# Optimization experiments

Hardware: AMD Instinct MI355X
Metric: run time of the kernel (lower is better)

Reference implementation:

```python
import jax, jax.numpy as jnp
import numpy as np

S, B, H, T = 512, 64, 512, 32

def setup_inputs() -> dict:
    key = jax.random.key(0)
    ks = jax.random.split(key, 6)
    hidden = jax.random.normal(ks[0], (S, B, H), jnp.float32)
    lens = jax.random.randint(ks[1], (B,), 1, S + 1)  # sentence lengths in [1, S]
    masks = jnp.ones((S, B), jnp.bool_)  # unused (attention is None), kept for signature parity
    W1 = jax.random.normal(ks[2], (H, H), jnp.float32) / np.sqrt(H)
    b1 = jnp.zeros((H,), jnp.float32)
    W2 = jax.random.normal(ks[3], (H, T), jnp.float32) / np.sqrt(H)
    b2 = jnp.zeros((T,), jnp.float32)
    # xavier_normal_ init for transition
    transition = jax.random.normal(ks[4], (T, T), jnp.float32) * np.sqrt(2.0 / (T + T))
    return {"hidden": hidden, "lens": lens, "masks": masks,
            "W1": W1, "b1": b1, "W2": W2, "b2": b2, "transition": transition}


def _viterbi(emissions, lens, transition):
    # emissions: [S, B, T]; transition[curr, prev]
    Sdim, Bdim, Tn = emissions.shape
    ident = jnp.broadcast_to(jnp.arange(Tn), (Bdim, Tn))  # identity backpointers for padded steps

    def step(fv, inp):
        em_t, t = inp
        scores = fv[:, None, :] + transition[None, :, :]  # [B, curr, prev]
        bp = jnp.argmax(scores, axis=-1)                  # [B, T]
        new_fv = jnp.max(scores, axis=-1) + em_t          # [B, T]
        active = (t < lens)[:, None]
        fv = jnp.where(active, new_fv, fv)                # freeze state past sentence end
        bp = jnp.where(active, bp, ident)
        return fv, bp

    fv0 = emissions[0]
    ts = jnp.arange(1, Sdim)
    fv, bps = jax.lax.scan(step, fv0, (emissions[1:], ts))  # bps: [S-1, B, T]
    best_id = jnp.argmax(fv, axis=-1)   # [B]
    best_score = jnp.max(fv, axis=-1)   # [B]

    def back(tag, bp_t):
        prev = jnp.take_along_axis(bp_t, tag[:, None], axis=1)[:, 0]
        return prev, prev

    _, prevs = jax.lax.scan(back, best_id, bps, reverse=True)  # [S-1, B]
    paths = jnp.concatenate([prevs, best_id[None]], axis=0)    # [S, B]; beyond len-1 the tag repeats
    return paths, best_score


def reference(hidden, lens, masks, W1, b1, W2, b2, transition):
    # hidden2emission: Linear -> Sigmoid -> Linear
    h1 = jax.nn.sigmoid(hidden @ W1 + b1)   # [S, B, H]
    emissions = h1 @ W2 + b2                # [S, B, T]
    paths, best_score = _viterbi(emissions, lens, transition)
    return paths, best_score
```

## Files before the change

### kernel.cpp

```cpp
#include <hip/hip_runtime.h>
#include <math.h>

#define SDIM 512
#define BDIM 64
#define HDIM 512
#define TDIM 32
#define MTOT (SDIM * BDIM)

typedef __attribute__((ext_vector_type(8))) short bf16x8;
typedef __attribute__((ext_vector_type(4))) float f32x4;

__device__ unsigned short g_w1hT[HDIM * HDIM];
__device__ unsigned short g_w1lT[HDIM * HDIM];
__device__ unsigned short g_w2hT[TDIM * HDIM];
__device__ unsigned short g_w2lT[TDIM * HDIM];
__device__ float g_em[(size_t)MTOT * TDIM];

__device__ __forceinline__ unsigned short f2bf(float x) {
  union { float f; unsigned int u; } v; v.f = x;
  unsigned int r = v.u + 0x7FFFu + ((v.u >> 16) & 1u);
  return (unsigned short)(r >> 16);
}
__device__ __forceinline__ float bf2f(unsigned short h) {
  union { float f; unsigned int u; } v; v.u = ((unsigned int)h) << 16; return v.f;
}
__device__ __forceinline__ float fmax3(float a, float b, float c) {
  return fmaxf(fmaxf(a, b), c);
}
__device__ __forceinline__ int imin3(int a, int b, int c) {
  int m = a < b ? a : b; return m < c ? m : c;
}

__global__ void split_kernel(const float* __restrict__ W1, const float* __restrict__ W2) {
  const int n = blockIdx.x;
  const int k0 = threadIdx.x * 4;
  if (n < HDIM) {
    ushort4 h, l; float x;
    x = W1[(size_t)(k0 + 0) * HDIM + n]; h.x = f2bf(x); l.x = f2bf(x - bf2f(h.x));
    x = W1[(size_t)(k0 + 1) * HDIM + n]; h.y = f2bf(x); l.y = f2bf(x - bf2f(h.y));
    x = W1[(size_t)(k0 + 2) * HDIM + n]; h.z = f2bf(x); l.z = f2bf(x - bf2f(h.z));
    x = W1[(size_t)(k0 + 3) * HDIM + n]; h.w = f2bf(x); l.w = f2bf(x - bf2f(h.w));
    *(ushort4*)&g_w1hT[(size_t)n * HDIM + k0] = h;
    *(ushort4*)&g_w1lT[(size_t)n * HDIM + k0] = l;
  } else {
    const int t = n - HDIM;
    ushort4 h, l; float x;
    x = W2[(size_t)(k0 + 0) * TDIM + t]; h.x = f2bf(x); l.x = f2bf(x - bf2f(h.x));
    x = W2[(size_t)(k0 + 1) * TDIM + t]; h.y = f2bf(x); l.y = f2bf(x - bf2f(h.y));
    x = W2[(size_t)(k0 + 2) * TDIM + t]; h.z = f2bf(x); l.z = f2bf(x - bf2f(h.z));
    x = W2[(size_t)(k0 + 3) * TDIM + t]; h.w = f2bf(x); l.w = f2bf(x - bf2f(h.w));
    *(ushort4*)&g_w2hT[(size_t)t * HDIM + k0] = h;
    *(ushort4*)&g_w2lT[(size_t)t * HDIM + k0] = l;
  }
}

__global__ __launch_bounds__(256) void emis_kernel(
    const float* __restrict__ hidden, const float* __restrict__ b1,
    const float* __restrict__ b2)
{
  __shared__ unsigned short lAh[64][40];
  __shared__ unsigned short lAl[64][40];
  __shared__ unsigned short lBh[128][40];
  __shared__ unsigned short lBl[128][40];
  __shared__ unsigned short H1h[64][136];
  __shared__ unsigned short H1l[64][136];

  const int tid = threadIdx.x;
  const int s = blockIdx.x;
  const int row0 = s * 64;
  const int wave = tid >> 6;
  const int lane = tid & 63;
  const int l15 = lane & 15;
  const int l4 = lane >> 4;
  const int wr1 = (wave >> 1) * 32;
  const int wc1 = (wave & 1) * 64;

  f32x4 acc_em[2];
  acc_em[0] = (f32x4)(0.f);
  acc_em[1] = (f32x4)(0.f);

  for (int jcb = 0; jcb < 4; ++jcb) {
    const int jc = jcb * 128;

    f32x4 acc1[2][4];
#pragma unroll
    for (int i = 0; i < 2; ++i)
#pragma unroll
      for (int j = 0; j < 4; ++j) acc1[i][j] = (f32x4)(0.f);

    for (int k0 = 0; k0 < HDIM; k0 += 32) {
#pragma unroll
      for (int i = 0; i < 2; ++i) {
        int f4 = tid + 256 * i;
        int r = f4 >> 3, q = f4 & 7;
        float4 v = *(const float4*)&hidden[(size_t)(row0 + r) * HDIM + k0 + 4 * q];
        ushort4 h, l;
        h.x = f2bf(v.x); l.x = f2bf(v.x - bf2f(h.x));
        h.y = f2bf(v.y); l.y = f2bf(v.y - bf2f(h.y));
        h.z = f2bf(v.z); l.z = f2bf(v.z - bf2f(h.z));
        h.w = f2bf(v.w); l.w = f2bf(v.w - bf2f(h.w));
        *(ushort4*)&lAh[r][4 * q] = h;
        *(ushort4*)&lAl[r][4 * q] = l;
      }
#pragma unroll
      for (int i = 0; i < 2; ++i) {
        int f8 = tid + 256 * i;
        int nl = f8 >> 2, kq8 = f8 & 3;
        *(uint4*)&lBh[nl][8 * kq8] =
            *(const uint4*)&g_w1hT[(size_t)(jc + nl) * HDIM + k0 + 8 * kq8];
        *(uint4*)&lBl[nl][8 * kq8] =
            *(const uint4*)&g_w1lT[(size_t)(jc + nl) * HDIM + k0 + 8 * kq8];
      }
      __syncthreads();

      bf16x8 aH[2], aL[2];
#pragma unroll
      for (int i = 0; i < 2; ++i) {
        aH[i] = *(const bf16x8*)&lAh[wr1 + 16 * i + l15][8 * l4];
        aL[i] = *(const bf16x8*)&lAl[wr1 + 16 * i + l15][8 * l4];
      }
#pragma unroll
      for (int j = 0; j < 4; ++j) {
        bf16x8 bH = *(const bf16x8*)&lBh[wc1 + 16 * j + l15][8 * l4];
        bf16x8 bL = *(const bf16x8*)&lBl[wc1 + 16 * j + l15][8 * l4];
#pragma unroll
        for (int i = 0; i < 2; ++i) {
          acc1[i][j] = __builtin_amdgcn_mfma_f32_16x16x32_bf16(aH[i], bH, acc1[i][j], 0, 0, 0);
          acc1[i][j] = __builtin_amdgcn_mfma_f32_16x16x32_bf16(aH[i], bL, acc1[i][j], 0, 0, 0);
          acc1[i][j] = __builtin_amdgcn_mfma_f32_16x16x32_bf16(aL[i], bH, acc1[i][j], 0, 0, 0);
        }
      }
      __syncthreads();
    }

#pragma unroll
    for (int j = 0; j < 4; ++j) {
      const int col = wc1 + 16 * j + l15;
      const float bv = b1[jc + col];
#pragma unroll
      for (int i = 0; i < 2; ++i) {
#pragma unroll
        for (int r = 0; r < 4; ++r) {
          int lrow = wr1 + 16 * i + 4 * l4 + r;
          float h = 1.f / (1.f + expf(-(acc1[i][j][r] + bv)));
          unsigned short hh = f2bf(h);
          unsigned short hl = f2bf(h - bf2f(hh));
          H1h[lrow][col] = hh;
          H1l[lrow][col] = hl;
        }
      }
    }
    __syncthreads();

#pragma unroll
    for (int ks = 0; ks < 4; ++ks) {
      bf16x8 aH2 = *(const bf16x8*)&H1h[16 * wave + l15][32 * ks + 8 * l4];
      bf16x8 aL2 = *(const bf16x8*)&H1l[16 * wave + l15][32 * ks + 8 * l4];
#pragma unroll
      for (int j2 = 0; j2 < 2; ++j2) {
        const size_t wo = (size_t)(16 * j2 + l15) * HDIM + jc + 32 * ks + 8 * l4;
        bf16x8 bH2 = *(const bf16x8*)&g_w2hT[wo];
        bf16x8 bL2 = *(const bf16x8*)&g_w2lT[wo];
        acc_em[j2] = __builtin_amdgcn_mfma_f32_16x16x32_bf16(aH2, bH2, acc_em[j2], 0, 0, 0);
        acc_em[j2] = __builtin_amdgcn_mfma_f32_16x16x32_bf16(aH2, bL2, acc_em[j2], 0, 0, 0);
        acc_em[j2] = __builtin_amdgcn_mfma_f32_16x16x32_bf16(aL2, bH2, acc_em[j2], 0, 0, 0);
      }
    }
    __syncthreads();
  }

#pragma unroll
  for (int j2 = 0; j2 < 2; ++j2) {
    const int t = 16 * j2 + l15;
    const float bv = b2[t];
#pragma unroll
    for (int r = 0; r < 4; ++r) {
      int b = 16 * wave + 4 * l4 + r;
      g_em[((size_t)b * SDIM + s) * TDIM + t] = acc_em[j2][r] + bv;
    }
  }
}

__global__ __launch_bounds__(64) void viterbi_kernel(
    const int* __restrict__ lens, const float* __restrict__ trans,
    float* __restrict__ out)
{
  __shared__ float fvL[64];
  __shared__ unsigned int bps32[SDIM / 4][TDIM];
  const int b = blockIdx.x;
  const int lane = threadIdx.x;
  const int c = lane & 31;
  const int h = lane >> 5;
  const int p0 = 16 * h;

  float tr[16];
#pragma unroll
  for (int j = 0; j < 16; j += 4) {
    float4 t4 = *(const float4*)&trans[c * TDIM + p0 + j];
    tr[j] = t4.x; tr[j + 1] = t4.y; tr[j + 2] = t4.z; tr[j + 3] = t4.w;
  }

  int len;
  { const int* p32 = lens;
    len = (p32[1] == 0) ? (int)((const long long*)lens)[b] : p32[b]; }

  const float* emc = g_em + (size_t)b * SDIM * TDIM + c;

  float fvown = emc[0];
  fvL[lane] = fvown;

  float ebuf[12];
#pragma unroll
  for (int j = 0; j < 12; ++j) ebuf[j] = emc[(size_t)(1 + j) * TDIM];

  unsigned int bpk = 0u;

#define VSTEP(T, PH, EV)                                                       \
  {                                                                            \
    float4 q0 = *(const float4*)&fvL[p0];                                      \
    float4 q1 = *(const float4*)&fvL[p0 + 4];                                  \
    float4 q2 = *(const float4*)&fvL[p0 + 8];                                  \
    float4 q3 = *(const float4*)&fvL[p0 + 12];                                 \
    float sv[16];                                                              \
    sv[0] = q0.x + tr[0];  sv[1] = q0.y + tr[1];                               \
    sv[2] = q0.z + tr[2];  sv[3] = q0.w + tr[3];                               \
    sv[4] = q1.x + tr[4];  sv[5] = q1.y + tr[5];                               \
    sv[6] = q1.z + tr[6];  sv[7] = q1.w + tr[7];                               \
    sv[8] = q2.x + tr[8];  sv[9] = q2.y + tr[9];                               \
    sv[10] = q2.z + tr[10]; sv[11] = q2.w + tr[11];                            \
    sv[12] = q3.x + tr[12]; sv[13] = q3.y + tr[13];                            \
    sv[14] = q3.z + tr[14]; sv[15] = q3.w + tr[15];                            \
    float l0 = fmax3(sv[0], sv[1], sv[2]);                                     \
    float l1 = fmax3(sv[3], sv[4], sv[5]);                                     \
    float l2 = fmax3(sv[6], sv[7], sv[8]);                                     \
    float l3 = fmax3(sv[9], sv[10], sv[11]);                                   \
    float l4 = fmax3(sv[12], sv[13], sv[14]);                                  \
    float mh = fmaxf(fmax3(l0, l1, l2), fmax3(l3, l4, sv[15]));                \
    float mo = __shfl_xor(mh, 32, 64);                                         \
    float m0 = fmaxf(mh, mo);                                                  \
    const bool act = (T) < len;                                                \
    fvown = act ? (m0 + (EV)) : fvown;                                         \
    fvL[lane] = fvown;       \
    int i_[16];                                                                \
    _Pragma("unroll")                                                          \
    for (int j = 0; j < 16; ++j) i_[j] = (sv[j] == m0) ? j : 63;               \
    int u0 = imin3(i_[0], i_[1], i_[2]);                                       \
    int u1 = imin3(i_[3], i_[4], i_[5]);                                       \
    int u2 = imin3(i_[6], i_[7], i_[8]);                                       \
    int u3 = imin3(i_[9], i_[10], i_[11]);                                     \
    int u4 = imin3(i_[12], i_[13], i_[14]);                                    \
    int jm = imin3(imin3(u0, u1, u2), imin3(u3, u4, i_[15]), 63);              \
    int gi = (jm == 63) ? 255 : (p0 + jm);                                     \
    int go = __shfl_xor(gi, 32, 64);                                           \
    int im = gi < go ? gi : go;                                                \
    int bp = act ? im : c;                                                     \
    bpk |= (unsigned)bp << (8 * (PH));                                         \
    if ((PH) == 3) { bps32[(T) >> 2][c] = bpk; bpk = 0u; }                     \
  }

#define LOADQ(BASE, T0)                                                        \
  {                                                                            \
    _Pragma("unroll")                                                          \
    for (int j = 0; j < 4; ++j) {                                              \
      int lt = (T0) + j; lt = lt > (SDIM - 1) ? (SDIM - 1) : lt;               \
      ebuf[(BASE) + j] = emc[(size_t)lt * TDIM];                               \
    }                                                                          \
  }

  {
    int tq = 1;
    for (; tq <= SDIM - 19; tq += 12) {
      VSTEP(tq + 0, 1, ebuf[0]) VSTEP(tq + 1, 2, ebuf[1])
      VSTEP(tq + 2, 3, ebuf[2]) VSTEP(tq + 3, 0, ebuf[3])
      LOADQ(0, tq + 12)
      VSTEP(tq + 4, 1, ebuf[4]) VSTEP(tq + 5, 2, ebuf[5])
      VSTEP(tq + 6, 3, ebuf[6]) VSTEP(tq + 7, 0, ebuf[7])
      LOADQ(4, tq + 16)
      VSTEP(tq + 8, 1, ebuf[8]) VSTEP(tq + 9, 2, ebuf[9])
      VSTEP(tq + 10, 3, ebuf[10]) VSTEP(tq + 11, 0, ebuf[11])
      LOADQ(8, tq + 20)
    }
    VSTEP(505, 1, ebuf[0]) VSTEP(506, 2, ebuf[1]) VSTEP(507, 3, ebuf[2])
    VSTEP(508, 0, ebuf[3]) VSTEP(509, 1, ebuf[4]) VSTEP(510, 2, ebuf[5])
    VSTEP(511, 3, ebuf[6])
  }
#undef VSTEP
#undef LOADQ

  float bs = fvown;
  int bi = c;
#pragma unroll
  for (int off = 16; off > 0; off >>= 1) {
    float os = __shfl_down(bs, off, 32);
    int oi = __shfl_down(bi, off, 32);
    if (os > bs || (os == bs && oi < bi)) { bs = os; bi = oi; }
  }
  bs = __shfl(bs, 0, 32);
  int tag = __shfl(bi, 0, 32);

  out[(size_t)SDIM * BDIM + b] = bs;
  out[(size_t)(SDIM - 1) * BDIM + b] = (float)tag;

  unsigned bw_next = bps32[SDIM / 4 - 1][c];
  for (int w = SDIM / 4 - 1; w >= 0; --w) {
    unsigned bw = bw_next;
    if (w > 0) bw_next = bps32[w - 1][c];
#pragma unroll
    for (int j = 3; j >= 0; --j) {
      int t = 4 * w + j;
      if (t < 1) continue;
      unsigned word = (unsigned)__builtin_amdgcn_readlane((int)bw, tag);
      tag = (int)((word >> (8 * j)) & 255u);
      out[(size_t)(t - 1) * BDIM + b] = (float)tag;
    }
  }
}

static int find_by_size(const int* in_sizes, int n_in, int sz, int fb) {
  for (int i = 0; i < n_in; ++i) if (in_sizes[i] == sz) return i;
  return fb;
}

extern "C" void kernel_launch(void* const* d_in, const int* in_sizes, int n_in,
                              void* d_out, int out_size, void* d_ws, size_t ws_size,
                              hipStream_t stream) {
  const int i_hidden = find_by_size(in_sizes, n_in, SDIM * BDIM * HDIM, 0);
  const int i_lens   = find_by_size(in_sizes, n_in, BDIM, 1);
  const int i_W1     = find_by_size(in_sizes, n_in, HDIM * HDIM, 3);
  const int i_b1     = find_by_size(in_sizes, n_in, HDIM, 4);
  const int i_W2     = find_by_size(in_sizes, n_in, HDIM * TDIM, 5);
  const int i_b2     = find_by_size(in_sizes, n_in, TDIM, 6);
  const int i_tr     = find_by_size(in_sizes, n_in, TDIM * TDIM, 7);

  const float* hidden = (const float*)d_in[i_hidden];
  const int*   lens   = (const int*)d_in[i_lens];
  const float* W1     = (const float*)d_in[i_W1];
  const float* b1     = (const float*)d_in[i_b1];
  const float* W2     = (const float*)d_in[i_W2];
  const float* b2     = (const float*)d_in[i_b2];
  const float* trans  = (const float*)d_in[i_tr];
  float* out = (float*)d_out;

  split_kernel<<<HDIM + TDIM, 128, 0, stream>>>(W1, W2);
  emis_kernel<<<SDIM, 256, 0, stream>>>(hidden, b1, b2);
  viterbi_kernel<<<BDIM, 64, 0, stream>>>(lens, trans, out);
}
```

Baseline: 239.4 us.

## Fuse emission GEMM and Viterbi into one kernel with per-timestep ready flags

Merges the emission kernel and the Viterbi kernel into a single launch. The first 512 blocks compute emissions per timestep and publish a per-timestep flag. Another 16 blocks each run four Viterbi waves that spin on those flags before loading emissions, so decoding overlaps the GEMM instead of waiting for it to finish. It also swaps expf for __expf. This relies on the Viterbi blocks not starving the producer blocks, since they are launched in the same grid, and it enlarges shared memory per block to 65KB, which may lower emission-block occupancy.

Result: slower. 519.2 us (+116.9%).

```diff
diff --git a/kernel.cpp b/kernel.cpp
--- a/kernel.cpp
+++ b/kernel.cpp
@@ -15,6 +15,7 @@
 __device__ unsigned short g_w2hT[TDIM * HDIM];
 __device__ unsigned short g_w2lT[TDIM * HDIM];
 __device__ float g_em[(size_t)MTOT * TDIM];
+__device__ unsigned int g_flag[SDIM];
 
 __device__ __forceinline__ unsigned short f2bf(float x) {
   union { float f; unsigned int u; } v; v.f = x;
@@ -29,6 +30,17 @@
 }
 __device__ __forceinline__ int imin3(int a, int b, int c) {
   int m = a < b ? a : b; return m < c ? m : c;
+}
+__device__ __forceinline__ void wait_flag(int s) {
+  while (__hip_atomic_load(&g_flag[s], __ATOMIC_ACQUIRE,
+                           __HIP_MEMORY_SCOPE_AGENT) == 0u) {
+    __builtin_amdgcn_s_sleep(2);
+  }
+}
+
+__global__ void init_flags() {
+  int i = blockIdx.x * blockDim.x + threadIdx.x;
+  if (i < SDIM) g_flag[i] = 0u;
 }
 
 __global__ void split_kernel(const float* __restrict__ W1, const float* __restrict__ W2) {
@@ -54,173 +66,184 @@
   }
 }
 
-__global__ __launch_bounds__(256) void emis_kernel(
+__global__ __launch_bounds__(256) void fused_kernel(
     const float* __restrict__ hidden, const float* __restrict__ b1,
-    const float* __restrict__ b2)
+    const float* __restrict__ b2, const int* __restrict__ lens,
+    const float* __restrict__ trans, float* __restrict__ out)
 {
-  __shared__ unsigned short lAh[64][40];
-  __shared__ unsigned short lAl[64][40];
-  __shared__ unsigned short lBh[128][40];
-  __shared__ unsigned short lBl[128][40];
-  __shared__ unsigned short H1h[64][136];
-  __shared__ unsigned short H1l[64][136];
-
-  const int tid = threadIdx.x;
-  const int s = blockIdx.x;
-  const int row0 = s * 64;
-  const int wave = tid >> 6;
-  const int lane = tid & 63;
-  const int l15 = lane & 15;
-  const int l4 = lane >> 4;
-  const int wr1 = (wave >> 1) * 32;
-  const int wc1 = (wave & 1) * 64;
-
-  f32x4 acc_em[2];
-  acc_em[0] = (f32x4)(0.f);
-  acc_em[1] = (f32x4)(0.f);
-
-  for (int jcb = 0; jcb < 4; ++jcb) {
-    const int jc = jcb * 128;
-
-    f32x4 acc1[2][4];
-#pragma unroll
-    for (int i = 0; i < 2; ++i)
-#pragma unroll
-      for (int j = 0; j < 4; ++j) acc1[i][j] = (f32x4)(0.f);
-
-    for (int k0 = 0; k0 < HDIM; k0 += 32) {
-#pragma unroll
-      for (int i = 0; i < 2; ++i) {
-        int f4 = tid + 256 * i;
-        int r = f4 >> 3, q = f4 & 7;
-        float4 v = *(const float4*)&hidden[(size_t)(row0 + r) * HDIM + k0 + 4 * q];
-        ushort4 h, l;
-        h.x = f2bf(v.x); l.x = f2bf(v.x - bf2f(h.x));
-        h.y = f2bf(v.y); l.y = f2bf(v.y - bf2f(h.y));
-        h.z = f2bf(v.z); l.z = f2bf(v.z - bf2f(h.z));
-        h.w = f2bf(v.w); l.w = f2bf(v.w - bf2f(h.w));
-        *(ushort4*)&lAh[r][4 * q] = h;
-        *(ushort4*)&lAl[r][4 * q] = l;
-      }
-#pragma unroll
-      for (int i = 0; i < 2; ++i) {
-        int f8 = tid + 256 * i;
-        int nl = f8 >> 2, kq8 = f8 & 3;
-        *(uint4*)&lBh[nl][8 * kq8] =
-            *(const uint4*)&g_w1hT[(size_t)(jc + nl) * HDIM + k0 + 8 * kq8];
-        *(uint4*)&lBl[nl][8 * kq8] =
-            *(const uint4*)&g_w1lT[(size_t)(jc + nl) * HDIM + k0 + 8 * kq8];
+  __shared__ __attribute__((aligned(16))) unsigned char raw[66560];
+
+  if (blockIdx.x < SDIM) {
+    unsigned short (*lAh)[40] = (unsigned short(*)[40])(raw + 0);
+    unsigned short (*lAl)[40] = (unsigned short(*)[40])(raw + 5120);
+    unsigned short (*lBh)[40] = (unsigned short(*)[40])(raw + 10240);
+    unsigned short (*lBl)[40] = (unsigned short(*)[40])(raw + 20480);
+    unsigned short (*H1h)[136] = (unsigned short(*)[136])(raw + 30720);
+    unsigned short (*H1l)[136] = (unsigned short(*)[136])(raw + 48128);
+
+    const int tid = threadIdx.x;
+    const int s = blockIdx.x;
+    const int row0 = s * 64;
+    const int wave = tid >> 6;
+    const int lane = tid & 63;
+    const int l15 = lane & 15;
+    const int l4 = lane >> 4;
+    const int wr1 = (wave >> 1) * 32;
+    const int wc1 = (wave & 1) * 64;
+
+    f32x4 acc_em[2];
+    acc_em[0] = (f32x4)(0.f);
+    acc_em[1] = (f32x4)(0.f);
+
+    for (int jcb = 0; jcb < 4; ++jcb) {
+      const int jc = jcb * 128;
+
+      f32x4 acc1[2][4];
+#pragma unroll
+      for (int i = 0; i < 2; ++i)
+#pragma unroll
+        for (int j = 0; j < 4; ++j) acc1[i][j] = (f32x4)(0.f);
+
+      for (int k0 = 0; k0 < HDIM; k0 += 32) {
+#pragma unroll
+        for (int i = 0; i < 2; ++i) {
+          int f4 = tid + 256 * i;
+          int r = f4 >> 3, q = f4 & 7;
+          float4 v = *(const float4*)&hidden[(size_t)(row0 + r) * HDIM + k0 + 4 * q];
+          ushort4 h, l;
+          h.x = f2bf(v.x); l.x = f2bf(v.x - bf2f(h.x));
+          h.y = f2bf(v.y); l.y = f2bf(v.y - bf2f(h.y));
+          h.z = f2bf(v.z); l.z = f2bf(v.z - bf2f(h.z));
+          h.w = f2bf(v.w); l.w = f2bf(v.w - bf2f(h.w));
+          *(ushort4*)&lAh[r][4 * q] = h;
+          *(ushort4*)&lAl[r][4 * q] = l;
+        }
+#pragma unroll
+        for (int i = 0; i < 2; ++i) {
+          int f8 = tid + 256 * i;
+          int nl = f8 >> 2, kq8 = f8 & 3;
+          *(uint4*)&lBh[nl][8 * kq8] =
+              *(const uint4*)&g_w1hT[(size_t)(jc + nl) * HDIM + k0 + 8 * kq8];
+          *(uint4*)&lBl[nl][8 * kq8] =
+              *(const uint4*)&g_w1lT[(size_t)(jc + nl) * HDIM + k0 + 8 * kq8];
+        }
+        __syncthreads();
+
+        bf16x8 aH[2], aL[2];
+#pragma unroll
+        for (int i = 0; i < 2; ++i) {
+          aH[i] = *(const bf16x8*)&lAh[wr1 + 16 * i + l15][8 * l4];
+          aL[i] = *(const bf16x8*)&lAl[wr1 + 16 * i + l15][8 * l4];
+        }
+#pragma unroll
+        for (int j = 0; j < 4; ++j) {
+          bf16x8 bH = *(const bf16x8*)&lBh[wc1 + 16 * j + l15][8 * l4];
+          bf16x8 bL = *(const bf16x8*)&lBl[wc1 + 16 * j + l15][8 * l4];
+#pragma unroll
+          for (int i = 0; i < 2; ++i) {
+            acc1[i][j] = __builtin_amdgcn_mfma_f32_16x16x32_bf16(aH[i], bH, acc1[i][j], 0, 0, 0);
+            acc1[i][j] = __builtin_amdgcn_mfma_f32_16x16x32_bf16(aH[i], bL, acc1[i][j], 0, 0, 0);
+            acc1[i][j] = __builtin_amdgcn_mfma_f32_16x16x32_bf16(aL[i], bH, acc1[i][j], 0, 0, 0);
+          }
+        }
+        __syncthreads();
+      }
+
+#pragma unroll
+      for (int j = 0; j < 4; ++j) {
+        const int col = wc1 + 16 * j + l15;
+        const float bv = b1[jc + col];
+#pragma unroll
+        for (int i = 0; i < 2; ++i) {
+#pragma unroll
+          for (int r = 0; r < 4; ++r) {
+            int lrow = wr1 + 16 * i + 4 * l4 + r;
+            float h = 1.f / (1.f + __expf(-(acc1[i][j][r] + bv)));
+            unsigned short hh = f2bf(h);
+            unsigned short hl = f2bf(h - bf2f(hh));
+            H1h[lrow][col] = hh;
+            H1l[lrow][col] = hl;
+          }
+        }
       }
       __syncthreads();
 
-      bf16x8 aH[2], aL[2];
-#pragma unroll
-      for (int i = 0; i < 2; ++i) {
-        aH[i] = *(const bf16x8*)&lAh[wr1 + 16 * i + l15][8 * l4];
-        aL[i] = *(const bf16x8*)&lAl[wr1 + 16 * i + l15][8 * l4];
-      }
-#pragma unroll
-      for (int j = 0; j < 4; ++j) {
-        bf16x8 bH = *(const bf16x8*)&lBh[wc1 + 16 * j + l15][8 * l4];
-        bf16x8 bL = *(const bf16x8*)&lBl[wc1 + 16 * j + l15][8 * l4];
-#pragma unroll
-        for (int i = 0; i < 2; ++i) {
-          acc1[i][j] = __builtin_amdgcn_mfma_f32_16x16x32_bf16(aH[i], bH, acc1[i][j], 0, 0, 0);
-          acc1[i][j] = __builtin_amdgcn_mfma_f32_16x16x32_bf16(aH[i], bL, acc1[i][j], 0, 0, 0);
-          acc1[i][j] = __builtin_amdgcn_mfma_f32_16x16x32_bf16(aL[i], bH, acc1[i][j], 0, 0, 0);
+#pragma unroll
+      for (int ks = 0; ks < 4; ++ks) {
+        bf16x8 aH2 = *(const bf16x8*)&H1h[16 * wave + l15][32 * ks + 8 * l4];
+        bf16x8 aL2 = *(const bf16x8*)&H1l[16 * wave + l15][32 * ks + 8 * l4];
+#pragma unroll
+        for (int j2 = 0; j2 < 2; ++j2) {
+          const size_t wo = (size_t)(16 * j2 + l15) * HDIM + jc + 32 * ks + 8 * l4;
+          bf16x8 bH2 = *(const bf16x8*)&g_w2hT[wo];
+          bf16x8 bL2 = *(const bf16x8*)&g_w2lT[wo];
+          acc_em[j2] = __builtin_amdgcn_mfma_f32_16x16x32_bf16(aH2, bH2, acc_em[j2], 0, 0, 0);
+          acc_em[j2] = __builtin_amdgcn_mfma_f32_16x16x32_bf16(aH2, bL2, acc_em[j2], 0, 0, 0);
+          acc_em[j2] = __builtin_amdgcn_mfma_f32_16x16x32_bf16(aL2, bH2, acc_em[j2], 0, 0, 0);
         }
       }
       __syncthreads();
     }
 
 #pragma unroll
-    for (int j = 0; j < 4; ++j) {
-      const int col = wc1 + 16 * j + l15;
-      const float bv = b1[jc + col];
-#pragma unroll
-      for (int i = 0; i < 2; ++i) {
-#pragma unroll
-        for (int r = 0; r < 4; ++r) {
-          int lrow = wr1 + 16 * i + 4 * l4 + r;
-          float h = 1.f / (1.f + expf(-(acc1[i][j][r] + bv)));
-          unsigned short hh = f2bf(h);
-          unsigned short hl = f2bf(h - bf2f(hh));
-          H1h[lrow][col] = hh;
-          H1l[lrow][col] = hl;
-        }
-      }
-    }
+    for (int j2 = 0; j2 < 2; ++j2) {
+      const int t = 16 * j2 + l15;
+      const float bv = b2[t];
+#pragma unroll
+      for (int r = 0; r < 4; ++r) {
+        int bb = 16 * wave + 4 * l4 + r;
+        g_em[((size_t)bb * SDIM + s) * TDIM + t] = acc_em[j2][r] + bv;
+      }
+    }
+
     __syncthreads();
-
-#pragma unroll
-    for (int ks = 0; ks < 4; ++ks) {
-      bf16x8 aH2 = *(const bf16x8*)&H1h[16 * wave + l15][32 * ks + 8 * l4];
-      bf16x8 aL2 = *(const bf16x8*)&H1l[16 * wave + l15][32 * ks + 8 * l4];
-#pragma unroll
-      for (int j2 = 0; j2 < 2; ++j2) {
-        const size_t wo = (size_t)(16 * j2 + l15) * HDIM + jc + 32 * ks + 8 * l4;
-        bf16x8 bH2 = *(const bf16x8*)&g_w2hT[wo];
-        bf16x8 bL2 = *(const bf16x8*)&g_w2lT[wo];
-        acc_em[j2] = __builtin_amdgcn_mfma_f32_16x16x32_bf16(aH2, bH2, acc_em[j2], 0, 0, 0);
-        acc_em[j2] = __builtin_amdgcn_mfma_f32_16x16x32_bf16(aH2, bL2, acc_em[j2], 0, 0, 0);
-        acc_em[j2] = __builtin_amdgcn_mfma_f32_16x16x32_bf16(aL2, bH2, acc_em[j2], 0, 0, 0);
-      }
-    }
-    __syncthreads();
-  }
-
-#pragma unroll
-  for (int j2 = 0; j2 < 2; ++j2) {
-    const int t = 16 * j2 + l15;
-    const float bv = b2[t];
-#pragma unroll
-    for (int r = 0; r < 4; ++r) {
-      int b = 16 * wave + 4 * l4 + r;
-      g_em[((size_t)b * SDIM + s) * TDIM + t] = acc_em[j2][r] + bv;
-    }
-  }
-}
-
-__global__ __launch_bounds__(64) void viterbi_kernel(
-    const int* __restrict__ lens, const float* __restrict__ trans,
-    float* __restrict__ out)
-{
-  __shared__ float fvL[64];
-  __shared__ unsigned int bps32[SDIM / 4][TDIM];
-  const int b = blockIdx.x;
-  const int lane = threadIdx.x;
-  const int c = lane & 31;
-  const int h = lane >> 5;
-  const int p0 = 16 * h;
-
-  float tr[16];
-#pragma unroll
-  for (int j = 0; j < 16; j += 4) {
-    float4 t4 = *(const float4*)&trans[c * TDIM + p0 + j];
-    tr[j] = t4.x; tr[j + 1] = t4.y; tr[j + 2] = t4.z; tr[j + 3] = t4.w;
-  }
-
-  int len;
-  { const int* p32 = lens;
-    len = (p32[1] == 0) ? (int)((const long long*)lens)[b] : p32[b]; }
-
-  const float* emc = g_em + (size_t)b * SDIM * TDIM + c;
-
-  float fvown = emc[0];
-  fvL[lane] = fvown;
-
-  float ebuf[12];
-#pragma unroll
-  for (int j = 0; j < 12; ++j) ebuf[j] = emc[(size_t)(1 + j) * TDIM];
-
-  unsigned int bpk = 0u;
+    if (tid == 0) {
+      __threadfence();
+      __hip_atomic_store(&g_flag[s], 1u, __ATOMIC_RELEASE, __HIP_MEMORY_SCOPE_AGENT);
+    }
+  } else {
+    unsigned int (*bpsw)[TDIM] =
+        (unsigned int(*)[TDIM])(raw + (size_t)(threadIdx.x >> 6) * (SDIM / 4) * TDIM * 4);
+    float* fvw = (float*)(raw + 65536) + (threadIdx.x >> 6) * 64;
+
+    const int tid = threadIdx.x;
+    const int wave = tid >> 6;
+    const int lane = tid & 63;
+    const int c = lane & 31;
+    const int h = lane >> 5;
+    const int p0 = 16 * h;
+    const int b = (blockIdx.x - SDIM) * 4 + wave;
+
+    float tr[16];
+#pragma unroll
+    for (int j = 0; j < 16; j += 4) {
+      float4 t4 = *(const float4*)&trans[c * TDIM + p0 + j];
+      tr[j] = t4.x; tr[j + 1] = t4.y; tr[j + 2] = t4.z; tr[j + 3] = t4.w;
+    }
+
+    int len;
+    { const int* p32 = lens;
+      len = (p32[1] == 0) ? (int)((const long long*)lens)[b] : p32[b]; }
+
+    const float* emc = g_em + (size_t)b * SDIM * TDIM + c;
+
+    for (int j = 0; j <= 12; ++j) wait_flag(j);
+
+    float fvown = emc[0];
+    fvw[lane] = fvown;
+
+    float ebuf[12];
+#pragma unroll
+    for (int j = 0; j < 12; ++j) ebuf[j] = emc[(size_t)(1 + j) * TDIM];
+
+    unsigned int bpk = 0u;
 
 #define VSTEP(T, PH, EV)                                                       \
   {                                                                            \
-    float4 q0 = *(const float4*)&fvL[p0];                                      \
-    float4 q1 = *(const float4*)&fvL[p0 + 4];                                  \
-    float4 q2 = *(const float4*)&fvL[p0 + 8];                                  \
-    float4 q3 = *(const float4*)&fvL[p0 + 12];                                 \
+    float4 q0 = *(const float4*)&fvw[p0];                                      \
+    float4 q1 = *(const float4*)&fvw[p0 + 4];                                  \
+    float4 q2 = *(const float4*)&fvw[p0 + 8];                                  \
+    float4 q3 = *(const float4*)&fvw[p0 + 12];                                 \
     float sv[16];                                                              \
     sv[0] = q0.x + tr[0];  sv[1] = q0.y + tr[1];                               \
     sv[2] = q0.z + tr[2];  sv[3] = q0.w + tr[3];                               \
@@ -240,7 +263,7 @@
     float m0 = fmaxf(mh, mo);                                                  \
     const bool act = (T) < len;                                                \
     fvown = act ? (m0 + (EV)) : fvown;                                         \
-    fvL[lane] = fvown;       \
+    fvw[lane] = fvown;                                                         \
     int i_[16];                                                                \
     _Pragma("unroll")                                                          \
     for (int j = 0; j < 16; ++j) i_[j] = (sv[j] == m0) ? j : 63;               \
@@ -255,7 +278,7 @@
     int im = gi < go ? gi : go;                                                \
     int bp = act ? im : c;                                                     \
     bpk |= (unsigned)bp << (8 * (PH));                                         \
-    if ((PH) == 3) { bps32[(T) >> 2][c] = bpk; bpk = 0u; }                     \
+    if ((PH) == 3) { bpsw[(T) >> 2][c] = bpk; bpk = 0u; }                      \
   }
 
 #define LOADQ(BASE, T0)                                                        \
@@ -263,55 +286,57 @@
     _Pragma("unroll")                                                          \
     for (int j = 0; j < 4; ++j) {                                              \
       int lt = (T0) + j; lt = lt > (SDIM - 1) ? (SDIM - 1) : lt;               \
+      wait_flag(lt);                                                           \
       ebuf[(BASE) + j] = emc[(size_t)lt * TDIM];                               \
     }                                                                          \
   }
 
-  {
-    int tq = 1;
-    for (; tq <= SDIM - 19; tq += 12) {
-      VSTEP(tq + 0, 1, ebuf[0]) VSTEP(tq + 1, 2, ebuf[1])
-      VSTEP(tq + 2, 3, ebuf[2]) VSTEP(tq + 3, 0, ebuf[3])
-      LOADQ(0, tq + 12)
-      VSTEP(tq + 4, 1, ebuf[4]) VSTEP(tq + 5, 2, ebuf[5])
-      VSTEP(tq + 6, 3, ebuf[6]) VSTEP(tq + 7, 0, ebuf[7])
-      LOADQ(4, tq + 16)
-      VSTEP(tq + 8, 1, ebuf[8]) VSTEP(tq + 9, 2, ebuf[9])
-      VSTEP(tq + 10, 3, ebuf[10]) VSTEP(tq + 11, 0, ebuf[11])
-      LOADQ(8, tq + 20)
-    }
-    VSTEP(505, 1, ebuf[0]) VSTEP(506, 2, ebuf[1]) VSTEP(507, 3, ebuf[2])
-    VSTEP(508, 0, ebuf[3]) VSTEP(509, 1, ebuf[4]) VSTEP(510, 2, ebuf[5])
-    VSTEP(511, 3, ebuf[6])
-  }
+    {
+      int tq = 1;
+      for (; tq <= SDIM - 19; tq += 12) {
+        VSTEP(tq + 0, 1, ebuf[0]) VSTEP(tq + 1, 2, ebuf[1])
+        VSTEP(tq + 2, 3, ebuf[2]) VSTEP(tq + 3, 0, ebuf[3])
+        LOADQ(0, tq + 12)
+        VSTEP(tq + 4, 1, ebuf[4]) VSTEP(tq + 5, 2, ebuf[5])
+        VSTEP(tq + 6, 3, ebuf[6]) VSTEP(tq + 7, 0, ebuf[7])
+        LOADQ(4, tq + 16)
+        VSTEP(tq + 8, 1, ebuf[8]) VSTEP(tq + 9, 2, ebuf[9])
+        VSTEP(tq + 10, 3, ebuf[10]) VSTEP(tq + 11, 0, ebuf[11])
+        LOADQ(8, tq + 20)
+      }
+      VSTEP(505, 1, ebuf[0]) VSTEP(506, 2, ebuf[1]) VSTEP(507, 3, ebuf[2])
+      VSTEP(508, 0, ebuf[3]) VSTEP(509, 1, ebuf[4]) VSTEP(510, 2, ebuf[5])
+      VSTEP(511, 3, ebuf[6])
+    }
 #undef VSTEP
 #undef LOADQ
 
-  float bs = fvown;
-  int bi = c;
-#pragma unroll
-  for (int off = 16; off > 0; off >>= 1) {
-    float os = __shfl_down(bs, off, 32);
-    int oi = __shfl_down(bi, off, 32);
-    if (os > bs || (os == bs && oi < bi)) { bs = os; bi = oi; }
-  }
-  bs = __shfl(bs, 0, 32);
-  int tag = __shfl(bi, 0, 32);
-
-  out[(size_t)SDIM * BDIM + b] = bs;
-  out[(size_t)(SDIM - 1) * BDIM + b] = (float)tag;
-
-  unsigned bw_next = bps32[SDIM / 4 - 1][c];
-  for (int w = SDIM / 4 - 1; w >= 0; --w) {
-    unsigned bw = bw_next;
-    if (w > 0) bw_next = bps32[w - 1][c];
-#pragma unroll
-    for (int j = 3; j >= 0; --j) {
-      int t = 4 * w + j;
-      if (t < 1) continue;
-      unsigned word = (unsigned)__builtin_amdgcn_readlane((int)bw, tag);
-      tag = (int)((word >> (8 * j)) & 255u);
-      out[(size_t)(t - 1) * BDIM + b] = (float)tag;
+    float bs = fvown;
+    int bi = c;
+#pragma unroll
+    for (int off = 16; off > 0; off >>= 1) {
+      float os = __shfl_down(bs, off, 32);
+      int oi = __shfl_down(bi, off, 32);
+      if (os > bs || (os == bs && oi < bi)) { bs = os; bi = oi; }
+    }
+    bs = __shfl(bs, 0, 32);
+    int tag = __shfl(bi, 0, 32);
+
+    out[(size_t)SDIM * BDIM + b] = bs;
+    out[(size_t)(SDIM - 1) * BDIM + b] = (float)tag;
+
+    unsigned bw_next = bpsw[SDIM / 4 - 1][c];
+    for (int w = SDIM / 4 - 1; w >= 0; --w) {
+      unsigned bw = bw_next;
+      if (w > 0) bw_next = bpsw[w - 1][c];
+#pragma unroll
+      for (int j = 3; j >= 0; --j) {
+        int t = 4 * w + j;
+        if (t < 1) continue;
+        unsigned word = (unsigned)__builtin_amdgcn_readlane((int)bw, tag);
+        tag = (int)((word >> (8 * j)) & 255u);
+        out[(size_t)(t - 1) * BDIM + b] = (float)tag;
+      }
     }
   }
 }
@@ -341,7 +366,7 @@
   const float* trans  = (const float*)d_in[i_tr];
   float* out = (float*)d_out;
 
+  init_flags<<<2, 256, 0, stream>>>();
   split_kernel<<<HDIM + TDIM, 128, 0, stream>>>(W1, W2);
-  emis_kernel<<<SDIM, 256, 0, stream>>>(hidden, b1, b2);
-  viterbi_kernel<<<BDIM, 64, 0, stream>>>(lens, trans, out);
-}
+  fused_kernel<<<SDIM + BDIM / 4, 256, 0, stream>>>(hidden, b1, b2, lens, trans, out);
+}
```
